# Optimization experiments

Measured on AMD Instinct MI355X. Metric: run time of the kernel, lower is better.

## Reference

```python
import jax, jax.numpy as jnp
import numpy as np
import math

EPS = 1e-5  # BatchNorm eps; eval mode with running_mean=0, running_var=1


def maxpool(x, k, p):
    return jax.lax.reduce_window(x, -jnp.inf, jax.lax.max,
                                 (1, 1, k, k), (1, 1, 1, 1),
                                 ((0, 0), (0, 0), (p, p), (p, p)))


def conv1x1(x, w, b=None):
    # x: [B,Cin,H,W], w: [Cout,Cin]
    y = jnp.einsum('oi,bihw->bohw', w, x)
    if b is not None:
        y = y + b[None, :, None, None]
    return y


def bn_eval(x, g, b):
    scale = g / jnp.sqrt(1.0 + EPS)
    return x * scale[None, :, None, None] + b[None, :, None, None]


def setup_inputs() -> dict:
    B, C, H, W = 2, 64, 80, 80
    c1, c2, c3 = 21, 21, 22
    ch = 32  # C//2
    ks = jax.random.split(jax.random.key(0), 16)
    s = 0.05
    inp = {
        'x': jax.random.normal(ks[0], (B, C, H, W), jnp.float32),
        'q1_w': jax.random.normal(ks[1], (c1, c1), jnp.float32) * s,
        'q1_g': jnp.ones((c1,), jnp.float32),
        'q1_b': jnp.zeros((c1,), jnp.float32),
        'q2_w': jax.random.normal(ks[2], (c2, c2), jnp.float32) * s,
        'q2_g': jnp.ones((c2,), jnp.float32),
        'q2_b': jnp.zeros((c2,), jnp.float32),
        'q3_w': jax.random.normal(ks[3], (c3, c3), jnp.float32) * s,
        'q3_g': jnp.ones((c3,), jnp.float32),
        'q3_b': jnp.zeros((c3,), jnp.float32),
        'k_hf_w': jax.random.normal(ks[4], (ch, C), jnp.float32) * s,
        'k_hf_b': jnp.zeros((ch,), jnp.float32),
        'k_lf_w': jax.random.normal(ks[5], (C - ch, C), jnp.float32) * s,
        'k_lf_b': jnp.zeros((C - ch,), jnp.float32),
        'k_fuse_w': jax.random.normal(ks[6], (C, C), jnp.float32) * s,
        'k_fuse_b': jnp.zeros((C,), jnp.float32),
        'v_bn_g': jnp.ones((C,), jnp.float32),
        'v_bn_b': jnp.zeros((C,), jnp.float32),
        'v_w': jax.random.normal(ks[7], (C, C), jnp.float32) * s,
        'v_b': jnp.zeros((C,), jnp.float32),
        'out_w': jax.random.normal(ks[8], (C, C), jnp.float32) * s,
        'out_b': jnp.zeros((C,), jnp.float32),
    }
    return inp


def reference(x, q1_w, q1_g, q1_b, q2_w, q2_g, q2_b, q3_w, q3_g, q3_b,
              k_hf_w, k_hf_b, k_lf_w, k_lf_b, k_fuse_w, k_fuse_b,
              v_bn_g, v_bn_b, v_w, v_b, out_w, out_b):
    B, C, H, W = x.shape
    N = H * W
    c1 = q1_w.shape[0]
    c2 = q2_w.shape[0]
    # Q: ThreeGroupConvQ (split -> 1x1 conv (no bias) -> BN -> ReLU -> concat)
    x1, x2, x3 = jnp.split(x, [c1, c1 + c2], axis=1)
    y1 = jax.nn.relu(bn_eval(conv1x1(x1, q1_w), q1_g, q1_b))
    y2 = jax.nn.relu(bn_eval(conv1x1(x2, q2_w), q2_g, q2_b))
    y3 = jax.nn.relu(bn_eval(conv1x1(x3, q3_w), q3_g, q3_b))
    Q = jnp.concatenate([y1, y2, y3], axis=1)
    # K: ThermalStructureExtractor
    p3 = maxpool(x, 3, 1)
    p5 = maxpool(x, 5, 2)
    low = (p3 + p5) * 0.5
    high = conv1x1(x - low, k_hf_w, k_hf_b)
    lowp = conv1x1(low, k_lf_w, k_lf_b)
    K = conv1x1(jnp.concatenate([high, lowp], axis=1), k_fuse_w, k_fuse_b)
    # V: BN -> 1x1 conv
    V = conv1x1(bn_eval(x, v_bn_g, v_bn_b), v_w, v_b)
    # attention over N = H*W spatial tokens, channel features
    Qc = Q.reshape(B, C, N)
    Kc = K.reshape(B, C, N)
    Vc = V.reshape(B, C, N)
    attn = jax.nn.softmax(
        jnp.einsum('bcn,bcm->bnm', Qc, Kc) / math.sqrt(C), axis=-1)  # [B,N,N]
    out = jnp.einsum('bnm,bcm->bcn', attn, Vc).reshape(B, C, H, W)
    return conv1x1(out, out_w, out_b) + x
```

## Files before the change

### kernel.cpp

```cpp
#include <hip/hip_runtime.h>
#include <hip/hip_bf16.h>


#define BATCH 2
#define CH 64
#define HH 80
#define WW 80
#define NN 6400
#define NT 100
#define KS 5
#define KTPS (NT/KS)
#define EPSV 1e-5f
#define NEGBIG (-1e30f)
#define LOG2E8 0.18033688f
#define VSP 65

typedef __hip_bfloat16 bf16;
typedef __attribute__((ext_vector_type(8))) short short8;
typedef __attribute__((ext_vector_type(4))) float f4;
#define MFMA16 __builtin_amdgcn_mfma_f32_16x16x32_bf16

__device__ __forceinline__ float b2f(bf16 v){ return __bfloat162float(v); }
__device__ __forceinline__ bf16 f2b(float v){ return __float2bfloat16(v); }
__device__ __forceinline__ ushort f2bu(float v){ return ((__hip_bfloat16_raw)__float2bfloat16(v)).x; }
__device__ __forceinline__ float bu2f(ushort u){
  union { unsigned int i; float f; } w; w.i = ((unsigned int)u) << 16; return w.f;
}
__device__ __forceinline__ unsigned pkbf(float a, float b){
  union { __hip_bfloat162 h2; unsigned u; } cv;
  cv.h2 = __float22bfloat162_rn(make_float2(a, b));
  return cv.u;
}
__device__ __forceinline__ float fexp2(float x){
#if __has_builtin(__builtin_amdgcn_exp2f)
  return __builtin_amdgcn_exp2f(x);
#else
  return exp2f(x);
#endif
}
__device__ __forceinline__ int swz(int row, int colb){
  return row*128 + (colb ^ ((row & 7) << 4));
}

#define OFF_BIAS 0
#define OFF_WH_B 768
#define OFF_LOW_B (768 + 32768)
#define OFF_Q_B   (OFF_LOW_B + BATCH*CH*NN*2)
#define OFF_K_B   (OFF_Q_B   + BATCH*CH*NN*2)
#define OFF_V_B   (OFF_K_B   + BATCH*CH*NN*2)
#define OFF_P_B   (OFF_V_B   + BATCH*CH*NN*2)
#define OFF_ML_B  (OFF_P_B   + BATCH*NT*KS*4096*2)

__global__ __launch_bounds__(256) void setup_fold(
    const float* __restrict__ q1w, const float* __restrict__ q1g, const float* __restrict__ q1b,
    const float* __restrict__ q2w, const float* __restrict__ q2g, const float* __restrict__ q2b,
    const float* __restrict__ q3w, const float* __restrict__ q3g, const float* __restrict__ q3b,
    const float* __restrict__ khw, const float* __restrict__ khb,
    const float* __restrict__ klw, const float* __restrict__ klb,
    const float* __restrict__ kfw, const float* __restrict__ kfb,
    const float* __restrict__ vg,  const float* __restrict__ vbnb,
    const float* __restrict__ vw,  const float* __restrict__ vb,
    const float* __restrict__ outw,
    float* __restrict__ biasf, bf16* __restrict__ wh)
{
  __shared__ __align__(16) float skf[4096];
  __shared__ __align__(16) float skh[2048];
  __shared__ __align__(16) float skl[2048];
  __shared__ __align__(16) float sow[4096];
  __shared__ __align__(16) float svw[4096];
  __shared__ float sbv[64];

  int tid = threadIdx.x;
  int blk = blockIdx.x;
  #pragma unroll
  for (int i = 0; i < 4; ++i) {
    *(float4*)&skf[(i*256 + tid)*4] = *(const float4*)&kfw[(i*256 + tid)*4];
    *(float4*)&sow[(i*256 + tid)*4] = *(const float4*)&outw[(i*256 + tid)*4];
    *(float4*)&svw[(i*256 + tid)*4] = *(const float4*)&vw[(i*256 + tid)*4];
  }
  #pragma unroll
  for (int i = 0; i < 2; ++i) {
    *(float4*)&skh[(i*256 + tid)*4] = *(const float4*)&khw[(i*256 + tid)*4];
    *(float4*)&skl[(i*256 + tid)*4] = *(const float4*)&klw[(i*256 + tid)*4];
  }
  __syncthreads();

  float rs = rsqrtf(1.0f + EPSV);
  if (tid < 64) {
    int j = tid;
    float bvo = vb[j];
    for (int ci2 = 0; ci2 < 64; ++ci2) bvo += svw[j*64 + ci2] * vbnb[ci2];
    sbv[j] = bvo;
  }

  bf16* wq   = wh;
  bf16* wvp  = wh + 4096;
  bf16* wa1  = wh + 8192;
  bf16* wa2m = wh + 12288;

  int t = blk*256 + tid;
  int ci = t & 63, co = t >> 6;
  int o = ci*64 + co;

  float w = 0.f, g;
  if (co < 21)      { g = q1g[co];    w = (ci < 21)              ? q1w[co*21 + ci]            : 0.f; }
  else if (co < 42) { g = q2g[co-21]; w = (ci >= 21 && ci < 42)  ? q2w[(co-21)*21 + (ci-21)]  : 0.f; }
  else              { g = q3g[co-42]; w = (ci >= 42)             ? q3w[(co-42)*22 + (ci-42)]  : 0.f; }
  wq[o] = f2b(w * g * rs * LOG2E8);

  float a1 = 0.f, a2 = 0.f;
  #pragma unroll
  for (int j = 0; j < 32; ++j) {
    a1 += skf[co*64 + j]      * skh[j*64 + ci];
    a2 += skf[co*64 + 32 + j] * skl[j*64 + ci];
  }
  wa1[o]  = f2b(a1);
  wa2m[o] = f2b(a2 - a1);

  float av = 0.f;
  #pragma unroll
  for (int j = 0; j < 64; ++j)
    av += sow[co*64 + j] * svw[j*64 + ci];
  wvp[o] = f2b(av * vg[ci] * rs);

  if (blk == 0 && tid < 64) {
    int c2 = tid;
    float bq;
    if (c2 < 21)      bq = q1b[c2];
    else if (c2 < 42) bq = q2b[c2-21];
    else              bq = q3b[c2-42];
    biasf[c2] = bq * LOG2E8;
    float bk = kfb[c2];
    #pragma unroll
    for (int j = 0; j < 32; ++j) {
      bk += skf[c2*64 + j]      * khb[j];
      bk += skf[c2*64 + 32 + j] * klb[j];
    }
    biasf[64 + c2] = bk;
    float bvp = 0.f;
    #pragma unroll
    for (int j = 0; j < 64; ++j) bvp += sow[c2*64 + j] * sbv[j];
    biasf[128 + c2] = bvp;
  }
}

__global__ __launch_bounds__(256) void pool_low(const float* __restrict__ x,
                                                bf16* __restrict__ lowg)
{
  int t4 = (blockIdx.x*256 + threadIdx.x)*4;
  int bc = t4 / NN; int n = t4 % NN;
  int h = n / WW, w0 = n % WW;
  const float* p = x + bc*NN;
  float m5[4], m3[4];
  #pragma unroll
  for (int j=0;j<4;++j){ m5[j]=NEGBIG; m3[j]=NEGBIG; }
  #pragma unroll
  for (int dh = -2; dh <= 2; ++dh) {
    int hh = h + dh; if (hh < 0 || hh >= HH) continue;
    float r[12];
    const float* row = p + hh*WW;
    if (w0 >= 4)      { float4 a = *(const float4*)&row[w0-4]; r[0]=a.x;r[1]=a.y;r[2]=a.z;r[3]=a.w; }
    else              { r[0]=NEGBIG;r[1]=NEGBIG;r[2]=NEGBIG;r[3]=NEGBIG; }
    { float4 a = *(const float4*)&row[w0]; r[4]=a.x;r[5]=a.y;r[6]=a.z;r[7]=a.w; }
    if (w0 + 7 < WW)  { float4 a = *(const float4*)&row[w0+4]; r[8]=a.x;r[9]=a.y;r[10]=a.z;r[11]=a.w; }
    else              { r[8]=NEGBIG;r[9]=NEGBIG;r[10]=NEGBIG;r[11]=NEGBIG; }
    bool in3 = (dh >= -1 && dh <= 1);
    #pragma unroll
    for (int j=0;j<4;++j) {
      float v3 = fmaxf(fmaxf(r[3+j], r[4+j]), r[5+j]);
      float v5 = fmaxf(fmaxf(r[2+j], v3), r[6+j]);
      m5[j] = fmaxf(m5[j], v5);
      if (in3) m3[j] = fmaxf(m3[j], v3);
    }
  }
  ushort4 o;
  o.x = f2bu(0.5f*(m3[0]+m5[0]));
  o.y = f2bu(0.5f*(m3[1]+m5[1]));
  o.z = f2bu(0.5f*(m3[2]+m5[2]));
  o.w = f2bu(0.5f*(m3[3]+m5[3]));
  *(ushort4*)&lowg[t4] = o;
}

__global__ __launch_bounds__(256) void qkv_kernel(
    const float* __restrict__ x, const float* __restrict__ biasf,
    const bf16* __restrict__ wh, const bf16* __restrict__ lowg,
    bf16* __restrict__ qgT, bf16* __restrict__ kgT, bf16* __restrict__ vgc)
{
  __shared__ __align__(16) float xs[64*32];
  __shared__ __align__(16) float lows[64*32];
  __shared__ __align__(16) bf16  wbuf[16384];
  __shared__ ushort vs[64*VSP];
  __shared__ float bias[192];

  int tid = threadIdx.x;
  int blk = blockIdx.x;
  int b = blk / (NT*2);
  int rem = blk % (NT*2);
  int tile = rem >> 1, half = rem & 1;
  int n0 = tile*64 + half*32;

  #pragma unroll
  for (int i = 0; i < 8; ++i) {
    int e = i*256 + tid; int c = e >> 5, p = e & 31;
    xs[c*32 + p]   = x[(b*CH + c)*NN + n0 + p];
    lows[c*32 + p] = b2f(lowg[(b*CH + c)*NN + n0 + p]);
  }
  #pragma unroll
  for (int i = 0; i < 16; ++i)
    ((uint2*)wbuf)[i*256 + tid] = ((const uint2*)wh)[i*256 + tid];
  if (tid < 192) bias[tid] = biasf[tid];
  __syncthreads();

  int co = tid & 63, pg = tid >> 6;
  const bf16* wq   = wbuf;
  const bf16* wvp  = wbuf + 4096;
  const bf16* wa1  = wbuf + 8192;
  const bf16* wa2m = wbuf + 12288;

  {
    float bq = bias[co];
    float4 a0 = make_float4(bq,bq,bq,bq), a1v = a0;
    for (int ci = 0; ci < 64; ++ci) {
      float wv = b2f(wq[ci*64 + co]);
      float4 x0 = *(const float4*)&xs[ci*32 + pg*8];
      float4 x1 = *(const float4*)&xs[ci*32 + pg*8 + 4];
      a0.x += wv*x0.x; a0.y += wv*x0.y; a0.z += wv*x0.z; a0.w += wv*x0.w;
      a1v.x += wv*x1.x; a1v.y += wv*x1.y; a1v.z += wv*x1.z; a1v.w += wv*x1.w;
    }
    float q8[8] = {a0.x,a0.y,a0.z,a0.w,a1v.x,a1v.y,a1v.z,a1v.w};
    #pragma unroll
    for (int j=0;j<8;++j)
      qgT[(size_t)(b*NN + n0 + pg*8 + j)*64 + co] = f2b(fmaxf(q8[j], 0.f));
  }
  {
    float bv = bias[128 + co];
    float4 a0 = make_float4(bv,bv,bv,bv), a1v = a0;
    for (int ci = 0; ci < 64; ++ci) {
      float wv = b2f(wvp[ci*64 + co]);
      float4 x0 = *(const float4*)&xs[ci*32 + pg*8];
      float4 x1 = *(const float4*)&xs[ci*32 + pg*8 + 4];
      a0.x += wv*x0.x; a0.y += wv*x0.y; a0.z += wv*x0.z; a0.w += wv*x0.w;
      a1v.x += wv*x1.x; a1v.y += wv*x1.y; a1v.z += wv*x1.z; a1v.w += wv*x1.w;
    }
    float v8[8] = {a0.x,a0.y,a0.z,a0.w,a1v.x,a1v.y,a1v.z,a1v.w};
    #pragma unroll
    for (int j=0;j<8;++j)
      vs[co*VSP + pg*8 + j] = f2bu(v8[j]);
  }
  __syncthreads();
  {
    int c = tid >> 2, cb = (tid & 3)*8;
    ushort u[8];
    #pragma unroll
    for (int j=0;j<8;++j) u[j] = vs[c*VSP + cb + j];
    uint4 pk;
    pk.x = (uint)u[0] | ((uint)u[1] << 16);
    pk.y = (uint)u[2] | ((uint)u[3] << 16);
    pk.z = (uint)u[4] | ((uint)u[5] << 16);
    pk.w = (uint)u[6] | ((uint)u[7] << 16);
    *(uint4*)&vgc[(size_t)(b*CH + c)*NN + n0 + cb] = pk;
  }
  {
    float bk = bias[64 + co];
    float4 a0 = make_float4(bk,bk,bk,bk), a1v = a0;
    for (int ci = 0; ci < 64; ++ci) {
      float w1 = b2f(wa1[ci*64 + co]);
      float w2 = b2f(wa2m[ci*64 + co]);
      float4 x0 = *(const float4*)&xs[ci*32 + pg*8];
      float4 x1 = *(const float4*)&xs[ci*32 + pg*8 + 4];
      float4 l0 = *(const float4*)&lows[ci*32 + pg*8];
      float4 l1 = *(const float4*)&lows[ci*32 + pg*8 + 4];
      a0.x += w1*x0.x + w2*l0.x; a0.y += w1*x0.y + w2*l0.y;
      a0.z += w1*x0.z + w2*l0.z; a0.w += w1*x0.w + w2*l0.w;
      a1v.x += w1*x1.x + w2*l1.x; a1v.y += w1*x1.y + w2*l1.y;
      a1v.z += w1*x1.z + w2*l1.z; a1v.w += w1*x1.w + w2*l1.w;
    }
    float k8[8] = {a0.x,a0.y,a0.z,a0.w,a1v.x,a1v.y,a1v.z,a1v.w};
    #pragma unroll
    for (int j=0;j<8;++j)
      kgT[(size_t)(b*NN + n0 + pg*8 + j)*64 + co] = f2b(k8[j]);
  }
}

__global__ __launch_bounds__(256, 2) void attn_partial(
    const bf16* __restrict__ qgT, const bf16* __restrict__ kgT, const bf16* __restrict__ vgc,
    ushort* __restrict__ part, float* __restrict__ pml)
{
  __shared__ __align__(16) char smem[32768];
  __shared__ float lred[256];

  int tid = threadIdx.x;
  int blk = blockIdx.x;
  int b = blk / (NT*KS);
  int rem = blk % (NT*KS);
  int tile = rem / KS, split = rem % KS;
  int n0 = tile*64;
  int wv = tid >> 6, lane = tid & 63, ln = lane & 15, quad = lane >> 4;
  int mbase = split*KTPS*64;

  int r0 = tid >> 3,         c0 = (tid & 7)*8;
  int r1 = 32 + (tid >> 3),  c1 = (tid & 7)*8;

  {
    uint4 qa = *(const uint4*)&qgT[(size_t)(b*NN + n0 + r0)*64 + c0];
    uint4 qb = *(const uint4*)&qgT[(size_t)(b*NN + n0 + r1)*64 + c1];
    *(uint4*)(smem + swz(r0, c0*2)) = qa;
    *(uint4*)(smem + swz(r1, c1*2)) = qb;
  }
  __syncthreads();
  short8 bq00 = *(const short8*)(smem + swz( 0*16 + ln, quad*16));
  short8 bq01 = *(const short8*)(smem + swz( 0*16 + ln, 64 + quad*16));
  short8 bq10 = *(const short8*)(smem + swz( 1*16 + ln, quad*16));
  short8 bq11 = *(const short8*)(smem + swz( 1*16 + ln, 64 + quad*16));
  short8 bq20 = *(const short8*)(smem + swz( 2*16 + ln, quad*16));
  short8 bq21 = *(const short8*)(smem + swz( 2*16 + ln, 64 + quad*16));
  short8 bq30 = *(const short8*)(smem + swz( 3*16 + ln, quad*16));
  short8 bq31 = *(const short8*)(smem + swz( 3*16 + ln, 64 + quad*16));
  {
    uint4 va  = *(const uint4*)&vgc[(size_t)(b*CH + r0)*NN + mbase + c0];
    uint4 vb4 = *(const uint4*)&vgc[(size_t)(b*CH + r1)*NN + mbase + c1];
    *(uint4*)(smem + 16384 + swz(r0, c0*2)) = va;
    *(uint4*)(smem + 16384 + swz(r1, c1*2)) = vb4;
  }
  const bf16* kb = kgT + (size_t)(b*NN + mbase + wv*16 + ln)*64;
  short8 ak0 = *(const short8*)&kb[quad*8];
  short8 ak1 = *(const short8*)&kb[32 + quad*8];
  __syncthreads();

  f4 accO0 = (f4){0.f,0.f,0.f,0.f};
  f4 accO1 = (f4){0.f,0.f,0.f,0.f};
  f4 accO2 = (f4){0.f,0.f,0.f,0.f};
  f4 accO3 = (f4){0.f,0.f,0.f,0.f};
  float lacc0 = 0.f, lacc1 = 0.f, lacc2 = 0.f, lacc3 = 0.f;

  uint4 vr0, vr1;
  short8 an0, an1;
  for (int kt = 0; kt < KTPS; ++kt) {
    const int po = (kt & 1) * 8192;
    const int vo = 16384 + (kt & 1) * 8192;
    {
      int ktn = (kt + 1 < KTPS) ? kt + 1 : kt;
      int m1 = mbase + ktn*64;
      vr0 = *(const uint4*)&vgc[(size_t)(b*CH + r0)*NN + m1 + c0];
      vr1 = *(const uint4*)&vgc[(size_t)(b*CH + r1)*NN + m1 + c1];
      an0 = *(const short8*)&kb[(size_t)ktn*4096 + quad*8];
      an1 = *(const short8*)&kb[(size_t)ktn*4096 + 32 + quad*8];
    }

    f4 accS0, accS1, accS2, accS3;
    {
      f4 z = (f4){0.f,0.f,0.f,0.f};
      z = MFMA16(ak0, bq00, z, 0, 0, 0);
      accS0 = MFMA16(ak1, bq01, z, 0, 0, 0);
    }
    {
      f4 z = (f4){0.f,0.f,0.f,0.f};
      z = MFMA16(ak0, bq10, z, 0, 0, 0);
      accS1 = MFMA16(ak1, bq11, z, 0, 0, 0);
    }
    {
      f4 z = (f4){0.f,0.f,0.f,0.f};
      z = MFMA16(ak0, bq20, z, 0, 0, 0);
      accS2 = MFMA16(ak1, bq21, z, 0, 0, 0);
    }
    {
      f4 z = (f4){0.f,0.f,0.f,0.f};
      z = MFMA16(ak0, bq30, z, 0, 0, 0);
      accS3 = MFMA16(ak1, bq31, z, 0, 0, 0);
    }
    {
      float p0 = fexp2(accS0[0]), p1 = fexp2(accS0[1]);
      float p2 = fexp2(accS0[2]), p3 = fexp2(accS0[3]);
      lacc0 += (p0 + p1) + (p2 + p3);
      uint2 pk; pk.x = pkbf(p0, p1); pk.y = pkbf(p2, p3);
      *(uint2*)(smem + po + swz(0*16 + ln, wv*32 + quad*8)) = pk;
    }
    {
      float p0 = fexp2(accS1[0]), p1 = fexp2(accS1[1]);
      float p2 = fexp2(accS1[2]), p3 = fexp2(accS1[3]);
      lacc1 += (p0 + p1) + (p2 + p3);
      uint2 pk; pk.x = pkbf(p0, p1); pk.y = pkbf(p2, p3);
      *(uint2*)(smem + po + swz(1*16 + ln, wv*32 + quad*8)) = pk;
    }
    {
      float p0 = fexp2(accS2[0]), p1 = fexp2(accS2[1]);
      float p2 = fexp2(accS2[2]), p3 = fexp2(accS2[3]);
      lacc2 += (p0 + p1) + (p2 + p3);
      uint2 pk; pk.x = pkbf(p0, p1); pk.y = pkbf(p2, p3);
      *(uint2*)(smem + po + swz(2*16 + ln, wv*32 + quad*8)) = pk;
    }
    {
      float p0 = fexp2(accS3[0]), p1 = fexp2(accS3[1]);
      float p2 = fexp2(accS3[2]), p3 = fexp2(accS3[3]);
      lacc3 += (p0 + p1) + (p2 + p3);
      uint2 pk; pk.x = pkbf(p0, p1); pk.y = pkbf(p2, p3);
      *(uint2*)(smem + po + swz(3*16 + ln, wv*32 + quad*8)) = pk;
    }
    __syncthreads();

    short8 ap0 = *(const short8*)(smem + po + swz(wv*16 + ln, quad*16));
    short8 ap1 = *(const short8*)(smem + po + swz(wv*16 + ln, 64 + quad*16));
    {
      short8 bv0 = *(const short8*)(smem + vo + swz(0*16 + ln, quad*16));
      short8 bv1 = *(const short8*)(smem + vo + swz(0*16 + ln, 64 + quad*16));
      accO0 = MFMA16(ap0, bv0, accO0, 0, 0, 0);
      accO0 = MFMA16(ap1, bv1, accO0, 0, 0, 0);
    }
    {
      short8 bv0 = *(const short8*)(smem + vo + swz(1*16 + ln, quad*16));
      short8 bv1 = *(const short8*)(smem + vo + swz(1*16 + ln, 64 + quad*16));
      accO1 = MFMA16(ap0, bv0, accO1, 0, 0, 0);
      accO1 = MFMA16(ap1, bv1, accO1, 0, 0, 0);
    }
    {
      short8 bv0 = *(const short8*)(smem + vo + swz(2*16 + ln, quad*16));
      short8 bv1 = *(const short8*)(smem + vo + swz(2*16 + ln, 64 + quad*16));
      accO2 = MFMA16(ap0, bv0, accO2, 0, 0, 0);
      accO2 = MFMA16(ap1, bv1, accO2, 0, 0, 0);
    }
    {
      short8 bv0 = *(const short8*)(smem + vo + swz(3*16 + ln, quad*16));
      short8 bv1 = *(const short8*)(smem + vo + swz(3*16 + ln, 64 + quad*16));
      accO3 = MFMA16(ap0, bv0, accO3, 0, 0, 0);
      accO3 = MFMA16(ap1, bv1, accO3, 0, 0, 0);
    }
    if (kt + 1 < KTPS) {
      int vn = 16384 + ((kt+1) & 1) * 8192;
      *(uint4*)(smem + vn + swz(r0, c0*2)) = vr0;
      *(uint4*)(smem + vn + swz(r1, c1*2)) = vr1;
    }
    ak0 = an0; ak1 = an1;
  }

  size_t pbase = ((size_t)(b*NT + tile)*KS + split)*4096;
  ushort* pp = part + pbase;
  {
    uint2 pk; pk.x = pkbf(accO0[0], accO0[1]); pk.y = pkbf(accO0[2], accO0[3]);
    *(uint2*)&pp[(0*16 + ln)*64 + wv*16 + quad*4] = pk;
  }
  {
    uint2 pk; pk.x = pkbf(accO1[0], accO1[1]); pk.y = pkbf(accO1[2], accO1[3]);
    *(uint2*)&pp[(1*16 + ln)*64 + wv*16 + quad*4] = pk;
  }
  {
    uint2 pk; pk.x = pkbf(accO2[0], accO2[1]); pk.y = pkbf(accO2[2], accO2[3]);
    *(uint2*)&pp[(2*16 + ln)*64 + wv*16 + quad*4] = pk;
  }
  {
    uint2 pk; pk.x = pkbf(accO3[0], accO3[1]); pk.y = pkbf(accO3[2], accO3[3]);
    *(uint2*)&pp[(3*16 + ln)*64 + wv*16 + quad*4] = pk;
  }
  {
    float s = lacc0;
    s += __shfl_xor(s, 16); s += __shfl_xor(s, 32);
    if (quad == 0) lred[wv*64 + 0*16 + ln] = s;
  }
  {
    float s = lacc1;
    s += __shfl_xor(s, 16); s += __shfl_xor(s, 32);
    if (quad == 0) lred[wv*64 + 1*16 + ln] = s;
  }
  {
    float s = lacc2;
    s += __shfl_xor(s, 16); s += __shfl_xor(s, 32);
    if (quad == 0) lred[wv*64 + 2*16 + ln] = s;
  }
  {
    float s = lacc3;
    s += __shfl_xor(s, 16); s += __shfl_xor(s, 32);
    if (quad == 0) lred[wv*64 + 3*16 + ln] = s;
  }
  __syncthreads();
  if (tid < 64) {
    size_t mlb = ((size_t)(b*NT + tile)*KS + split)*64;
    pml[mlb + tid] = (lred[tid] + lred[64 + tid]) + (lred[128 + tid] + lred[192 + tid]);
  }
}

__global__ __launch_bounds__(256) void attn_reduce(
    const ushort* __restrict__ part, const float* __restrict__ pml,
    const float* __restrict__ x, const float* __restrict__ outb,
    float* __restrict__ out)
{
  __shared__ float linv[64];
  __shared__ float ob[64];

  int tid = threadIdx.x;
  int blk = blockIdx.x;
  int b = blk / NT, tile = blk % NT;
  size_t base = (size_t)(b*NT + tile)*KS;

  if (tid < 64) {
    float l = 0.f;
    #pragma unroll
    for (int s=0;s<KS;++s) l += pml[(base+s)*64 + tid];
    linv[tid] = 1.0f / l;
    ob[tid] = outb[tid];
  }
  __syncthreads();

  #pragma unroll
  for (int j = 0; j < 4; ++j) {
    int idx = j*256 + tid;
    int c = idx >> 4, q = idx & 15;
    float a0=0.f, a1=0.f, a2=0.f, a3=0.f;
    #pragma unroll
    for (int s = 0; s < KS; ++s) {
      uint2 v = *(const uint2*)&part[(base+s)*4096 + (size_t)c*64 + q*4];
      a0 += bu2f((ushort)(v.x & 0xffff)); a1 += bu2f((ushort)(v.x >> 16));
      a2 += bu2f((ushort)(v.y & 0xffff)); a3 += bu2f((ushort)(v.y >> 16));
    }
    int nl = q*4;
    size_t gidx = (size_t)(b*CH + c)*NN + tile*64 + nl;
    float4 xv = *(const float4*)&x[gidx];
    float bc = ob[c];
    float4 o;
    o.x = a0*linv[nl+0] + bc + xv.x;
    o.y = a1*linv[nl+1] + bc + xv.y;
    o.z = a2*linv[nl+2] + bc + xv.z;
    o.w = a3*linv[nl+3] + bc + xv.w;
    *(float4*)&out[gidx] = o;
  }
}

extern "C" void kernel_launch(void* const* d_in, const int* in_sizes, int n_in,
                              void* d_out, int out_size, void* d_ws, size_t ws_size,
                              hipStream_t stream) {
  const float* x    = (const float*)d_in[0];
  const float* q1w  = (const float*)d_in[1];
  const float* q1g  = (const float*)d_in[2];
  const float* q1b  = (const float*)d_in[3];
  const float* q2w  = (const float*)d_in[4];
  const float* q2g  = (const float*)d_in[5];
  const float* q2b  = (const float*)d_in[6];
  const float* q3w  = (const float*)d_in[7];
  const float* q3g  = (const float*)d_in[8];
  const float* q3b  = (const float*)d_in[9];
  const float* khw  = (const float*)d_in[10];
  const float* khb  = (const float*)d_in[11];
  const float* klw  = (const float*)d_in[12];
  const float* klb  = (const float*)d_in[13];
  const float* kfw  = (const float*)d_in[14];
  const float* kfb  = (const float*)d_in[15];
  const float* vbg  = (const float*)d_in[16];
  const float* vbb  = (const float*)d_in[17];
  const float* vw   = (const float*)d_in[18];
  const float* vb   = (const float*)d_in[19];
  const float* outw = (const float*)d_in[20];
  const float* outb = (const float*)d_in[21];

  char*   wsb  = (char*)d_ws;
  float*  biasf= (float*)(wsb + OFF_BIAS);
  bf16*   wh   = (bf16*)(wsb + OFF_WH_B);
  bf16*   lowg = (bf16*)(wsb + OFF_LOW_B);
  bf16*   qgT  = (bf16*)(wsb + OFF_Q_B);
  bf16*   kgT  = (bf16*)(wsb + OFF_K_B);
  bf16*   vgc  = (bf16*)(wsb + OFF_V_B);
  ushort* part = (ushort*)(wsb + OFF_P_B);
  float*  pml  = (float*)(wsb + OFF_ML_B);

  hipLaunchKernelGGL(setup_fold, dim3(16), dim3(256), 0, stream,
                     q1w,q1g,q1b,q2w,q2g,q2b,q3w,q3g,q3b,
                     khw,khb,klw,klb,kfw,kfb,vbg,vbb,vw,vb,outw, biasf, wh);
  hipLaunchKernelGGL(pool_low, dim3(BATCH*CH*NN/1024), dim3(256), 0, stream, x, lowg);
  hipLaunchKernelGGL(qkv_kernel, dim3(BATCH*NT*2), dim3(256), 0, stream,
                     x, biasf, wh, lowg, qgT, kgT, vgc);
  hipLaunchKernelGGL(attn_partial, dim3(BATCH*NT*KS), dim3(256), 0, stream,
                     qgT, kgT, vgc, part, pml);
  hipLaunchKernelGGL(attn_reduce, dim3(BATCH*NT), dim3(256), 0, stream,
                     part, pml, x, outb, (float*)d_out);
}
```

Measured before the change: 153.8 us.

## Compute Q/K/V projections with bf16 MFMA instead of scalar FMA loops

Rewrites the QKV projection kernel so the 1x1 convolutions run on 16x16x32 bf16 MFMA instructions. Inputs are staged into swizzled transposed LDS tiles, and the folded weights are stored co-major so they can be read straight from global memory. The grid is halved to 64-token tiles, and the V transpose through LDS is removed by writing MFMA fragments directly. In exchange, x is rounded to bf16 before the matmul, which slightly lowers precision, and fewer blocks are launched.

```diff
diff --git a/kernel.cpp b/kernel.cpp
--- a/kernel.cpp
+++ b/kernel.cpp
@@ -13,7 +13,6 @@
 #define EPSV 1e-5f
 #define NEGBIG (-1e30f)
 #define LOG2E8 0.18033688f
-#define VSP 65
 
 typedef __hip_bfloat16 bf16;
 typedef __attribute__((ext_vector_type(8))) short short8;
@@ -100,7 +99,7 @@
 
   int t = blk*256 + tid;
   int ci = t & 63, co = t >> 6;
-  int o = ci*64 + co;
+  int o = co*64 + ci;
 
   float w = 0.f, g;
   if (co < 21)      { g = q1g[co];    w = (ci < 21)              ? q1w[co*21 + ci]            : 0.f; }
@@ -181,104 +180,215 @@
   *(ushort4*)&lowg[t4] = o;
 }
 
-__global__ __launch_bounds__(256) void qkv_kernel(
+__global__ __launch_bounds__(256, 2) void qkv_kernel(
     const float* __restrict__ x, const float* __restrict__ biasf,
     const bf16* __restrict__ wh, const bf16* __restrict__ lowg,
     bf16* __restrict__ qgT, bf16* __restrict__ kgT, bf16* __restrict__ vgc)
 {
-  __shared__ __align__(16) float xs[64*32];
-  __shared__ __align__(16) float lows[64*32];
-  __shared__ __align__(16) bf16  wbuf[16384];
-  __shared__ ushort vs[64*VSP];
+  __shared__ __align__(16) char xT[8192];
+  __shared__ __align__(16) char lT[8192];
   __shared__ float bias[192];
 
   int tid = threadIdx.x;
   int blk = blockIdx.x;
-  int b = blk / (NT*2);
-  int rem = blk % (NT*2);
-  int tile = rem >> 1, half = rem & 1;
-  int n0 = tile*64 + half*32;
-
-  #pragma unroll
-  for (int i = 0; i < 8; ++i) {
-    int e = i*256 + tid; int c = e >> 5, p = e & 31;
-    xs[c*32 + p]   = x[(b*CH + c)*NN + n0 + p];
-    lows[c*32 + p] = b2f(lowg[(b*CH + c)*NN + n0 + p]);
-  }
-  #pragma unroll
-  for (int i = 0; i < 16; ++i)
-    ((uint2*)wbuf)[i*256 + tid] = ((const uint2*)wh)[i*256 + tid];
+  int b = blk / NT, tile = blk % NT;
+  int n0 = tile*64;
+  int wv = tid >> 6, lane = tid & 63, ln = lane & 15, quad = lane >> 4;
+
   if (tid < 192) bias[tid] = biasf[tid];
+
+  {
+    int cq = tid & 15, nq = tid >> 4;
+    const float* xp = x + (size_t)(b*CH + cq*4)*NN + n0 + nq*4;
+    float4 x0 = *(const float4*)&xp[0*NN];
+    float4 x1 = *(const float4*)&xp[(size_t)1*NN];
+    float4 x2 = *(const float4*)&xp[(size_t)2*NN];
+    float4 x3 = *(const float4*)&xp[(size_t)3*NN];
+    const bf16* lp = lowg + (size_t)(b*CH + cq*4)*NN + n0 + nq*4;
+    uint2 l0 = *(const uint2*)&lp[0*NN];
+    uint2 l1 = *(const uint2*)&lp[(size_t)1*NN];
+    uint2 l2 = *(const uint2*)&lp[(size_t)2*NN];
+    uint2 l3 = *(const uint2*)&lp[(size_t)3*NN];
+    uint2 w;
+    w.x = pkbf(x0.x, x1.x); w.y = pkbf(x2.x, x3.x);
+    *(uint2*)(xT + swz(nq*4+0, cq*8)) = w;
+    w.x = (l0.x & 0xffffu) | ((l1.x & 0xffffu) << 16);
+    w.y = (l2.x & 0xffffu) | ((l3.x & 0xffffu) << 16);
+    *(uint2*)(lT + swz(nq*4+0, cq*8)) = w;
+    w.x = pkbf(x0.y, x1.y); w.y = pkbf(x2.y, x3.y);
+    *(uint2*)(xT + swz(nq*4+1, cq*8)) = w;
+    w.x = (l0.x >> 16) | ((l1.x >> 16) << 16);
+    w.y = (l2.x >> 16) | ((l3.x >> 16) << 16);
+    *(uint2*)(lT + swz(nq*4+1, cq*8)) = w;
+    w.x = pkbf(x0.z, x1.z); w.y = pkbf(x2.z, x3.z);
+    *(uint2*)(xT + swz(nq*4+2, cq*8)) = w;
+    w.x = (l0.y & 0xffffu) | ((l1.y & 0xffffu) << 16);
+    w.y = (l2.y & 0xffffu) | ((l3.y & 0xffffu) << 16);
+    *(uint2*)(lT + swz(nq*4+2, cq*8)) = w;
+    w.x = pkbf(x0.w, x1.w); w.y = pkbf(x2.w, x3.w);
+    *(uint2*)(xT + swz(nq*4+3, cq*8)) = w;
+    w.x = (l0.y >> 16) | ((l1.y >> 16) << 16);
+    w.y = (l2.y >> 16) | ((l3.y >> 16) << 16);
+    *(uint2*)(lT + swz(nq*4+3, cq*8)) = w;
+  }
   __syncthreads();
 
-  int co = tid & 63, pg = tid >> 6;
-  const bf16* wq   = wbuf;
-  const bf16* wvp  = wbuf + 4096;
-  const bf16* wa1  = wbuf + 8192;
-  const bf16* wa2m = wbuf + 12288;
-
-  {
-    float bq = bias[co];
-    float4 a0 = make_float4(bq,bq,bq,bq), a1v = a0;
-    for (int ci = 0; ci < 64; ++ci) {
-      float wv = b2f(wq[ci*64 + co]);
-      float4 x0 = *(const float4*)&xs[ci*32 + pg*8];
-      float4 x1 = *(const float4*)&xs[ci*32 + pg*8 + 4];
-      a0.x += wv*x0.x; a0.y += wv*x0.y; a0.z += wv*x0.z; a0.w += wv*x0.w;
-      a1v.x += wv*x1.x; a1v.y += wv*x1.y; a1v.z += wv*x1.z; a1v.w += wv*x1.w;
-    }
-    float q8[8] = {a0.x,a0.y,a0.z,a0.w,a1v.x,a1v.y,a1v.z,a1v.w};
-    #pragma unroll
-    for (int j=0;j<8;++j)
-      qgT[(size_t)(b*NN + n0 + pg*8 + j)*64 + co] = f2b(fmaxf(q8[j], 0.f));
-  }
-  {
-    float bv = bias[128 + co];
-    float4 a0 = make_float4(bv,bv,bv,bv), a1v = a0;
-    for (int ci = 0; ci < 64; ++ci) {
-      float wv = b2f(wvp[ci*64 + co]);
-      float4 x0 = *(const float4*)&xs[ci*32 + pg*8];
-      float4 x1 = *(const float4*)&xs[ci*32 + pg*8 + 4];
-      a0.x += wv*x0.x; a0.y += wv*x0.y; a0.z += wv*x0.z; a0.w += wv*x0.w;
-      a1v.x += wv*x1.x; a1v.y += wv*x1.y; a1v.z += wv*x1.z; a1v.w += wv*x1.w;
-    }
-    float v8[8] = {a0.x,a0.y,a0.z,a0.w,a1v.x,a1v.y,a1v.z,a1v.w};
-    #pragma unroll
-    for (int j=0;j<8;++j)
-      vs[co*VSP + pg*8 + j] = f2bu(v8[j]);
-  }
-  __syncthreads();
-  {
-    int c = tid >> 2, cb = (tid & 3)*8;
-    ushort u[8];
-    #pragma unroll
-    for (int j=0;j<8;++j) u[j] = vs[c*VSP + cb + j];
-    uint4 pk;
-    pk.x = (uint)u[0] | ((uint)u[1] << 16);
-    pk.y = (uint)u[2] | ((uint)u[3] << 16);
-    pk.z = (uint)u[4] | ((uint)u[5] << 16);
-    pk.w = (uint)u[6] | ((uint)u[7] << 16);
-    *(uint4*)&vgc[(size_t)(b*CH + c)*NN + n0 + cb] = pk;
-  }
-  {
-    float bk = bias[64 + co];
-    float4 a0 = make_float4(bk,bk,bk,bk), a1v = a0;
-    for (int ci = 0; ci < 64; ++ci) {
-      float w1 = b2f(wa1[ci*64 + co]);
-      float w2 = b2f(wa2m[ci*64 + co]);
-      float4 x0 = *(const float4*)&xs[ci*32 + pg*8];
-      float4 x1 = *(const float4*)&xs[ci*32 + pg*8 + 4];
-      float4 l0 = *(const float4*)&lows[ci*32 + pg*8];
-      float4 l1 = *(const float4*)&lows[ci*32 + pg*8 + 4];
-      a0.x += w1*x0.x + w2*l0.x; a0.y += w1*x0.y + w2*l0.y;
-      a0.z += w1*x0.z + w2*l0.z; a0.w += w1*x0.w + w2*l0.w;
-      a1v.x += w1*x1.x + w2*l1.x; a1v.y += w1*x1.y + w2*l1.y;
-      a1v.z += w1*x1.z + w2*l1.z; a1v.w += w1*x1.w + w2*l1.w;
-    }
-    float k8[8] = {a0.x,a0.y,a0.z,a0.w,a1v.x,a1v.y,a1v.z,a1v.w};
-    #pragma unroll
-    for (int j=0;j<8;++j)
-      kgT[(size_t)(b*NN + n0 + pg*8 + j)*64 + co] = f2b(k8[j]);
+  short8 xb00 = *(const short8*)(xT + swz(0*16 + ln, quad*16));
+  short8 xb01 = *(const short8*)(xT + swz(0*16 + ln, 64 + quad*16));
+  short8 xb10 = *(const short8*)(xT + swz(1*16 + ln, quad*16));
+  short8 xb11 = *(const short8*)(xT + swz(1*16 + ln, 64 + quad*16));
+  short8 xb20 = *(const short8*)(xT + swz(2*16 + ln, quad*16));
+  short8 xb21 = *(const short8*)(xT + swz(2*16 + ln, 64 + quad*16));
+  short8 xb30 = *(const short8*)(xT + swz(3*16 + ln, quad*16));
+  short8 xb31 = *(const short8*)(xT + swz(3*16 + ln, 64 + quad*16));
+  short8 xa0 = *(const short8*)(xT + swz(wv*16 + ln, quad*16));
+  short8 xa1 = *(const short8*)(xT + swz(wv*16 + ln, 64 + quad*16));
+
+  int cb = wv*16 + quad*4;
+  const bf16* wqp  = wh;
+  const bf16* wvpp = wh + 4096;
+  const bf16* wa1p = wh + 8192;
+  const bf16* wa2p = wh + 12288;
+  int wrow = (wv*16 + ln)*64;
+
+  {
+    {
+      short8 w0 = *(const short8*)&wvpp[(0*16 + ln)*64 + quad*8];
+      short8 w1 = *(const short8*)&wvpp[(0*16 + ln)*64 + 32 + quad*8];
+      float bv = bias[128 + 0*16 + ln];
+      f4 a = (f4){bv, bv, bv, bv};
+      a = MFMA16(xa0, w0, a, 0, 0, 0);
+      a = MFMA16(xa1, w1, a, 0, 0, 0);
+      uint2 pk; pk.x = pkbf(a[0], a[1]); pk.y = pkbf(a[2], a[3]);
+      *(uint2*)&vgc[(size_t)(b*CH + 0*16 + ln)*NN + n0 + cb] = pk;
+    }
+    {
+      short8 w0 = *(const short8*)&wvpp[(1*16 + ln)*64 + quad*8];
+      short8 w1 = *(const short8*)&wvpp[(1*16 + ln)*64 + 32 + quad*8];
+      float bv = bias[128 + 1*16 + ln];
+      f4 a = (f4){bv, bv, bv, bv};
+      a = MFMA16(xa0, w0, a, 0, 0, 0);
+      a = MFMA16(xa1, w1, a, 0, 0, 0);
+      uint2 pk; pk.x = pkbf(a[0], a[1]); pk.y = pkbf(a[2], a[3]);
+      *(uint2*)&vgc[(size_t)(b*CH + 1*16 + ln)*NN + n0 + cb] = pk;
+    }
+    {
+      short8 w0 = *(const short8*)&wvpp[(2*16 + ln)*64 + quad*8];
+      short8 w1 = *(const short8*)&wvpp[(2*16 + ln)*64 + 32 + quad*8];
+      float bv = bias[128 + 2*16 + ln];
+      f4 a = (f4){bv, bv, bv, bv};
+      a = MFMA16(xa0, w0, a, 0, 0, 0);
+      a = MFMA16(xa1, w1, a, 0, 0, 0);
+      uint2 pk; pk.x = pkbf(a[0], a[1]); pk.y = pkbf(a[2], a[3]);
+      *(uint2*)&vgc[(size_t)(b*CH + 2*16 + ln)*NN + n0 + cb] = pk;
+    }
+    {
+      short8 w0 = *(const short8*)&wvpp[(3*16 + ln)*64 + quad*8];
+      short8 w1 = *(const short8*)&wvpp[(3*16 + ln)*64 + 32 + quad*8];
+      float bv = bias[128 + 3*16 + ln];
+      f4 a = (f4){bv, bv, bv, bv};
+      a = MFMA16(xa0, w0, a, 0, 0, 0);
+      a = MFMA16(xa1, w1, a, 0, 0, 0);
+      uint2 pk; pk.x = pkbf(a[0], a[1]); pk.y = pkbf(a[2], a[3]);
+      *(uint2*)&vgc[(size_t)(b*CH + 3*16 + ln)*NN + n0 + cb] = pk;
+    }
+  }
+
+  {
+    short8 wq0 = *(const short8*)&wqp[wrow + quad*8];
+    short8 wq1 = *(const short8*)&wqp[wrow + 32 + quad*8];
+    f4 bQ;
+    bQ[0] = bias[cb+0]; bQ[1] = bias[cb+1]; bQ[2] = bias[cb+2]; bQ[3] = bias[cb+3];
+    {
+      f4 a = bQ;
+      a = MFMA16(wq0, xb00, a, 0, 0, 0);
+      a = MFMA16(wq1, xb01, a, 0, 0, 0);
+      uint2 pk;
+      pk.x = pkbf(fmaxf(a[0],0.f), fmaxf(a[1],0.f));
+      pk.y = pkbf(fmaxf(a[2],0.f), fmaxf(a[3],0.f));
+      *(uint2*)&qgT[(size_t)(b*NN + n0 + 0*16 + ln)*64 + cb] = pk;
+    }
+    {
+      f4 a = bQ;
+      a = MFMA16(wq0, xb10, a, 0, 0, 0);
+      a = MFMA16(wq1, xb11, a, 0, 0, 0);
+      uint2 pk;
+      pk.x = pkbf(fmaxf(a[0],0.f), fmaxf(a[1],0.f));
+      pk.y = pkbf(fmaxf(a[2],0.f), fmaxf(a[3],0.f));
+      *(uint2*)&qgT[(size_t)(b*NN + n0 + 1*16 + ln)*64 + cb] = pk;
+    }
+    {
+      f4 a = bQ;
+      a = MFMA16(wq0, xb20, a, 0, 0, 0);
+      a = MFMA16(wq1, xb21, a, 0, 0, 0);
+      uint2 pk;
+      pk.x = pkbf(fmaxf(a[0],0.f), fmaxf(a[1],0.f));
+      pk.y = pkbf(fmaxf(a[2],0.f), fmaxf(a[3],0.f));
+      *(uint2*)&qgT[(size_t)(b*NN + n0 + 2*16 + ln)*64 + cb] = pk;
+    }
+    {
+      f4 a = bQ;
+      a = MFMA16(wq0, xb30, a, 0, 0, 0);
+      a = MFMA16(wq1, xb31, a, 0, 0, 0);
+      uint2 pk;
+      pk.x = pkbf(fmaxf(a[0],0.f), fmaxf(a[1],0.f));
+      pk.y = pkbf(fmaxf(a[2],0.f), fmaxf(a[3],0.f));
+      *(uint2*)&qgT[(size_t)(b*NN + n0 + 3*16 + ln)*64 + cb] = pk;
+    }
+  }
+
+  {
+    short8 wa10 = *(const short8*)&wa1p[wrow + quad*8];
+    short8 wa11 = *(const short8*)&wa1p[wrow + 32 + quad*8];
+    short8 wm0  = *(const short8*)&wa2p[wrow + quad*8];
+    short8 wm1  = *(const short8*)&wa2p[wrow + 32 + quad*8];
+    short8 lb00 = *(const short8*)(lT + swz(0*16 + ln, quad*16));
+    short8 lb01 = *(const short8*)(lT + swz(0*16 + ln, 64 + quad*16));
+    short8 lb10 = *(const short8*)(lT + swz(1*16 + ln, quad*16));
+    short8 lb11 = *(const short8*)(lT + swz(1*16 + ln, 64 + quad*16));
+    short8 lb20 = *(const short8*)(lT + swz(2*16 + ln, quad*16));
+    short8 lb21 = *(const short8*)(lT + swz(2*16 + ln, 64 + quad*16));
+    short8 lb30 = *(const short8*)(lT + swz(3*16 + ln, quad*16));
+    short8 lb31 = *(const short8*)(lT + swz(3*16 + ln, 64 + quad*16));
+    f4 bK;
+    bK[0] = bias[64+cb+0]; bK[1] = bias[64+cb+1];
+    bK[2] = bias[64+cb+2]; bK[3] = bias[64+cb+3];
+    {
+      f4 a = bK;
+      a = MFMA16(wa10, xb00, a, 0, 0, 0);
+      a = MFMA16(wa11, xb01, a, 0, 0, 0);
+      a = MFMA16(wm0,  lb00, a, 0, 0, 0);
+      a = MFMA16(wm1,  lb01, a, 0, 0, 0);
+      uint2 pk; pk.x = pkbf(a[0], a[1]); pk.y = pkbf(a[2], a[3]);
+      *(uint2*)&kgT[(size_t)(b*NN + n0 + 0*16 + ln)*64 + cb] = pk;
+    }
+    {
+      f4 a = bK;
+      a = MFMA16(wa10, xb10, a, 0, 0, 0);
+      a = MFMA16(wa11, xb11, a, 0, 0, 0);
+      a = MFMA16(wm0,  lb10, a, 0, 0, 0);
+      a = MFMA16(wm1,  lb11, a, 0, 0, 0);
+      uint2 pk; pk.x = pkbf(a[0], a[1]); pk.y = pkbf(a[2], a[3]);
+      *(uint2*)&kgT[(size_t)(b*NN + n0 + 1*16 + ln)*64 + cb] = pk;
+    }
+    {
+      f4 a = bK;
+      a = MFMA16(wa10, xb20, a, 0, 0, 0);
+      a = MFMA16(wa11, xb21, a, 0, 0, 0);
+      a = MFMA16(wm0,  lb20, a, 0, 0, 0);
+      a = MFMA16(wm1,  lb21, a, 0, 0, 0);
+      uint2 pk; pk.x = pkbf(a[0], a[1]); pk.y = pkbf(a[2], a[3]);
+      *(uint2*)&kgT[(size_t)(b*NN + n0 + 2*16 + ln)*64 + cb] = pk;
+    }
+    {
+      f4 a = bK;
+      a = MFMA16(wa10, xb30, a, 0, 0, 0);
+      a = MFMA16(wa11, xb31, a, 0, 0, 0);
+      a = MFMA16(wm0,  lb30, a, 0, 0, 0);
+      a = MFMA16(wm1,  lb31, a, 0, 0, 0);
+      uint2 pk; pk.x = pkbf(a[0], a[1]); pk.y = pkbf(a[2], a[3]);
+      *(uint2*)&kgT[(size_t)(b*NN + n0 + 3*16 + ln)*64 + cb] = pk;
+    }
   }
 }
 
@@ -563,7 +673,7 @@
                      q1w,q1g,q1b,q2w,q2g,q2b,q3w,q3g,q3b,
                      khw,khb,klw,klb,kfw,kfb,vbg,vbb,vw,vb,outw, biasf, wh);
   hipLaunchKernelGGL(pool_low, dim3(BATCH*CH*NN/1024), dim3(256), 0, stream, x, lowg);
-  hipLaunchKernelGGL(qkv_kernel, dim3(BATCH*NT*2), dim3(256), 0, stream,
+  hipLaunchKernelGGL(qkv_kernel, dim3(BATCH*NT), dim3(256), 0, stream,
                      x, biasf, wh, lowg, qgT, kgT, vgc);
   hipLaunchKernelGGL(attn_partial, dim3(BATCH*NT*KS), dim3(256), 0, stream,
                      qgT, kgT, vgc, part, pml);
```

New measurement: 147.9 us. 1.04x faster.
